# Kernel tuning notes

Hardware: AMD Instinct MI355X
Metric: run time of the kernel (lower is better)

## Reference

```python
import jax, jax.numpy as jnp
import numpy as np

N_NODES = 100000
N_EDGES = 1600000
D_IN = 128
D_OUT = 128
EPS = 1e-5


def setup_inputs() -> dict:
    key = jax.random.key(0)
    ks = jax.random.split(key, 5)
    x = jax.random.normal(ks[0], (N_NODES, D_IN), dtype=jnp.float32)
    edge_index = jax.random.randint(ks[1], (2, N_EDGES), 0, N_NODES, dtype=jnp.int64)
    scale = 1.0 / np.sqrt(D_IN)
    W_root = jax.random.normal(ks[2], (D_IN, D_OUT), dtype=jnp.float32) * scale
    W_rel = jax.random.normal(ks[3], (D_IN, D_OUT), dtype=jnp.float32) * scale
    b_rel = jax.random.normal(ks[4], (D_OUT,), dtype=jnp.float32) * 0.01
    gamma = jnp.ones((D_OUT,), dtype=jnp.float32)
    beta = jnp.zeros((D_OUT,), dtype=jnp.float32)
    return {"x": x, "edge_index": edge_index, "W_root": W_root, "W_rel": W_rel,
            "b_rel": b_rel, "gamma": gamma, "beta": beta}


def reference(x, edge_index, W_root, W_rel, b_rel, gamma, beta):
    # GraphConv: out = aggr(x_j) @ W_rel + b_rel + x @ W_root   (aggr = sum)
    src = edge_index[0]
    dst = edge_index[1]
    aggr = jax.ops.segment_sum(x[src], dst, num_segments=x.shape[0])  # [N, D_IN]
    h = aggr @ W_rel + b_rel + x @ W_root                              # [N, D_OUT]
    # NodeLevelBatchNorm (training mode: batch stats over node dim, biased var)
    mean = jnp.mean(h, axis=0)
    var = jnp.mean(jnp.square(h - mean), axis=0)
    h_norm = (h - mean) * jax.lax.rsqrt(var + EPS) * gamma + beta
    return jax.nn.relu(h_norm)
```

## Files before the change

### kernel.cpp

```cpp
#include <hip/hip_runtime.h>

#define N_NODES 100000
#define N_EDGES 1600000
#define D 128
#define NB 196
#define EPT 10
#define CHUNK 2560
#define BIN_BLOCKS 625
#define CVT_X_BLOCKS 6250
#define ZROW N_NODES

typedef __bf16 bf16x8 __attribute__((ext_vector_type(8)));
typedef float f32x4 __attribute__((ext_vector_type(4)));

__device__ __forceinline__ unsigned f2bf(float f) {
    unsigned u = __float_as_uint(f);
    return (u + 0x7fffu + ((u >> 16) & 1u)) >> 16;
}
__device__ __forceinline__ float bf_lo(unsigned u) { return __uint_as_float(u << 16); }
__device__ __forceinline__ float bf_hi(unsigned u) { return __uint_as_float(u & 0xffff0000u); }

__global__ __launch_bounds__(256) void prep_kernel(const float* __restrict__ x,
                                                   const float* __restrict__ Wrel,
                                                   const float* __restrict__ Wroot,
                                                   const int* __restrict__ ei,
                                                   unsigned short* __restrict__ x_bf,
                                                   unsigned short* __restrict__ Wt,
                                                   int* __restrict__ bcount) {
    __shared__ int h[256];
    int b = blockIdx.x;
    int t = threadIdx.x;
    if (b < CVT_X_BLOCKS) {
        size_t i = ((size_t)b * 256 + t) * 8;
        float4 v0 = *(const float4*)(x + i);
        float4 v1 = *(const float4*)(x + i + 4);
        uint4 p;
        p.x = f2bf(v0.x) | (f2bf(v0.y) << 16);
        p.y = f2bf(v0.z) | (f2bf(v0.w) << 16);
        p.z = f2bf(v1.x) | (f2bf(v1.y) << 16);
        p.w = f2bf(v1.z) | (f2bf(v1.w) << 16);
        *(uint4*)(x_bf + i) = p;
    } else if (b < CVT_X_BLOCKS + 128) {
        int c = b - CVT_X_BLOCKS;
        float v = (t < 128) ? Wrel[t * D + c] : Wroot[(t - 128) * D + c];
        Wt[c * 256 + t] = (unsigned short)f2bf(v);
    } else if (b == CVT_X_BLOCKS + 128) {
        if (t < 16) *(uint4*)(x_bf + (size_t)ZROW * D + t * 8) = make_uint4(0, 0, 0, 0);
    } else {
        int blk = b - (CVT_X_BLOCKS + 129);
        h[t] = 0;
        __syncthreads();
        int base = blk * CHUNK;
#pragma unroll
        for (int i = 0; i < EPT; ++i) {
            int dst = ei[N_EDGES + base + i * 256 + t];
            atomicAdd(&h[dst >> 9], 1);
        }
        __syncthreads();
        if (t < NB && h[t]) atomicAdd(&bcount[t], h[t]);
    }
}

__global__ __launch_bounds__(256) void bscan_kernel(const int* __restrict__ bcount,
                                                    int* __restrict__ bucket_base,
                                                    int* __restrict__ bcur) {
    __shared__ int s[256];
    int t = threadIdx.x;
    int v = (t < NB) ? bcount[t] : 0;
    s[t] = v;
    __syncthreads();
    for (int off = 1; off < 256; off <<= 1) {
        int a = (t >= off) ? s[t - off] : 0;
        __syncthreads();
        s[t] += a;
        __syncthreads();
    }
    int excl = s[t] - v;
    if (t < NB) {
        bucket_base[t] = excl;
        bcur[t] = excl;
    }
    if (t == NB) bucket_base[NB] = N_EDGES;
}

__global__ __launch_bounds__(256) void binify_kernel(const int* __restrict__ ei,
                                                     int* __restrict__ bcur,
                                                     unsigned* __restrict__ epk) {
    __shared__ int lhist[256];
    __shared__ int lstart[256];
    __shared__ int lfill[256];
    __shared__ int gbase[256];
    __shared__ uint2 stage[CHUNK];

    int t = threadIdx.x;
    int base = blockIdx.x * CHUNK;
    lhist[t] = 0;
    lfill[t] = 0;
    __syncthreads();

    int src[EPT], dst[EPT];
#pragma unroll
    for (int i = 0; i < EPT; ++i) {
        int e = base + i * 256 + t;
        src[i] = ei[e];
        dst[i] = ei[N_EDGES + e];
        atomicAdd(&lhist[dst[i] >> 9], 1);
    }
    __syncthreads();

    int v = lhist[t];
    lstart[t] = v;
    __syncthreads();
    for (int off = 1; off < 256; off <<= 1) {
        int a = (t >= off) ? lstart[t - off] : 0;
        __syncthreads();
        lstart[t] += a;
        __syncthreads();
    }
    int excl = lstart[t] - v;
    if (t < NB && v > 0) gbase[t] = atomicAdd(&bcur[t], v);
    __syncthreads();
    lstart[t] = excl;
    __syncthreads();

#pragma unroll
    for (int i = 0; i < EPT; ++i) {
        int b = dst[i] >> 9;
        int lp = atomicAdd(&lfill[b], 1);
        stage[lstart[b] + lp] = make_uint2((unsigned)src[i], (unsigned)dst[i]);
    }
    __syncthreads();

    for (int i = t; i < CHUNK; i += 256) {
        uint2 p = stage[i];
        int b = (int)(p.y >> 9);
        unsigned code = p.x | ((p.y & 511u) << 17);
        epk[gbase[b] + (i - lstart[b])] = code;
    }
}

__global__ __launch_bounds__(256) void place_kernel(const unsigned* __restrict__ epk,
                                                    const int* __restrict__ bucket_base,
                                                    int* __restrict__ rowstart,
                                                    int* __restrict__ srcs) {
    __shared__ int bufA[512];
    __shared__ int bufB[512];
    int b = blockIdx.x;
    int t = threadIdx.x;
    int pbeg = bucket_base[b];
    int pend = bucket_base[b + 1];

    bufA[t] = 0;
    bufA[t + 256] = 0;
    __syncthreads();
    for (int i = pbeg + t; i < pend; i += 256)
        atomicAdd(&bufA[epk[i] >> 17], 1);
    __syncthreads();

    for (int j = t; j < 512; j += 256) bufB[j] = j ? bufA[j - 1] : 0;
    __syncthreads();
    int* cur = bufB;
    int* nxt = bufA;
    for (int off = 1; off < 512; off <<= 1) {
        for (int j = t; j < 512; j += 256)
            nxt[j] = cur[j] + ((j >= off) ? cur[j - off] : 0);
        __syncthreads();
        int* tmp = cur; cur = nxt; nxt = tmp;
    }

    for (int j = t; j < 512; j += 256) {
        int gnode = (b << 9) + j;
        int val = pbeg + cur[j];
        if (gnode <= N_NODES) rowstart[gnode] = val;
        nxt[j] = val;
    }
    __syncthreads();

    for (int i = pbeg + t; i < pend; i += 256) {
        unsigned code = epk[i];
        int pos = atomicAdd(&nxt[code >> 17], 1);
        srcs[pos] = (int)(code & 0x1FFFFu);
    }
}

__global__ __launch_bounds__(256) void gather_kernel(const unsigned short* __restrict__ x_bf,
                                                     const int* __restrict__ rowstart,
                                                     const int* __restrict__ srcs,
                                                     unsigned short* __restrict__ aggr_bf) {
    int t = threadIdx.x;
    int node = blockIdx.x * 16 + (t >> 4);
    int l16 = t & 15;
    int begin = rowstart[node];
    int end = rowstart[node + 1];
    const unsigned short* xp = x_bf + l16 * 8;
    float a0 = 0.f, a1 = 0.f, a2 = 0.f, a3 = 0.f;
    float a4 = 0.f, a5 = 0.f, a6 = 0.f, a7 = 0.f;
    for (int e = begin; e < end; e += 8) {
        int idx[8];
#pragma unroll
        for (int i = 0; i < 8; ++i) {
            int ee = e + i;
            int ec = (ee < end) ? ee : (end - 1);
            int sv = srcs[ec];
            idx[i] = (ee < end) ? sv : ZROW;
        }
        uint4 u[8];
#pragma unroll
        for (int i = 0; i < 8; ++i) u[i] = *(const uint4*)(xp + (size_t)idx[i] * D);
#pragma unroll
        for (int i = 0; i < 8; ++i) {
            a0 += bf_lo(u[i].x);
            a1 += bf_hi(u[i].x);
            a2 += bf_lo(u[i].y);
            a3 += bf_hi(u[i].y);
            a4 += bf_lo(u[i].z);
            a5 += bf_hi(u[i].z);
            a6 += bf_lo(u[i].w);
            a7 += bf_hi(u[i].w);
        }
    }
    uint4 w;
    w.x = f2bf(a0) | (f2bf(a1) << 16);
    w.y = f2bf(a2) | (f2bf(a3) << 16);
    w.z = f2bf(a4) | (f2bf(a5) << 16);
    w.w = f2bf(a6) | (f2bf(a7) << 16);
    *(uint4*)(aggr_bf + (size_t)node * D + l16 * 8) = w;
}

__global__ __launch_bounds__(256) void gemm_mfma(const unsigned short* __restrict__ aggr_bf,
                                                 const unsigned short* __restrict__ x_bf,
                                                 const unsigned short* __restrict__ Wt,
                                                 const float* __restrict__ brel,
                                                 unsigned short* __restrict__ h_bf,
                                                 float* __restrict__ gsum,
                                                 float* __restrict__ gss) {
    __shared__ unsigned short Bf[2048 * 8];
    __shared__ float sbias[128];
    __shared__ float SredS[4][128];
    __shared__ float SredQ[4][128];

    const int t = threadIdx.x;
    const int wave = t >> 6;
    const int lane = t & 63;
    const int quad = lane >> 4;
    const int l16 = lane & 15;
    const int blockRow = blockIdx.x * 128;

    if (t < 128) sbias[t] = brel[t];

    f32x4 acc[2][8];
#pragma unroll
    for (int i = 0; i < 2; ++i)
#pragma unroll
        for (int j = 0; j < 8; ++j) acc[i][j] = (f32x4){0.f, 0.f, 0.f, 0.f};

    const int rowb = blockRow + wave * 32;

#pragma unroll
    for (int half = 0; half < 2; ++half) {
#pragma unroll
        for (int f = t; f < 2048; f += 256) {
            int kcl = f >> 9;
            int ct = (f >> 6) & 7;
            int ln = f & 63;
            int col = ct * 16 + (ln & 15);
            int kb = half * 128 + kcl * 32 + ((ln >> 4) << 3);
            *(uint4*)&Bf[f * 8] = *(const uint4*)(Wt + col * 256 + kb);
        }
        __syncthreads();

        const unsigned short* Asrc = half ? x_bf : aggr_bf;
#pragma unroll
        for (int kcl = 0; kcl < 4; ++kcl) {
            const int k0 = kcl * 32 + quad * 8;
            bf16x8 af0 = *(const bf16x8*)(Asrc + (size_t)(rowb + l16) * D + k0);
            bf16x8 af1 = *(const bf16x8*)(Asrc + (size_t)(rowb + 16 + l16) * D + k0);
#pragma unroll
            for (int ct = 0; ct < 8; ++ct) {
                bf16x8 bfrag = *(const bf16x8*)&Bf[((kcl * 8 + ct) * 64 + lane) * 8];
                acc[0][ct] = __builtin_amdgcn_mfma_f32_16x16x32_bf16(af0, bfrag, acc[0][ct], 0, 0, 0);
                acc[1][ct] = __builtin_amdgcn_mfma_f32_16x16x32_bf16(af1, bfrag, acc[1][ct], 0, 0, 0);
            }
        }
        if (half == 0) __syncthreads();
    }

    float csum[8], css[8];
#pragma unroll
    for (int ct = 0; ct < 8; ++ct) { csum[ct] = 0.f; css[ct] = 0.f; }

#pragma unroll
    for (int rt = 0; rt < 2; ++rt) {
#pragma unroll
        for (int ct = 0; ct < 8; ++ct) {
            int col = ct * 16 + l16;
            float bv = sbias[col];
#pragma unroll
            for (int reg = 0; reg < 4; ++reg) {
                int row = blockRow + wave * 32 + rt * 16 + quad * 4 + reg;
                if (row < N_NODES) {
                    float v = acc[rt][ct][reg] + bv;
                    h_bf[(size_t)row * D + col] = (unsigned short)f2bf(v);
                    csum[ct] += v;
                    css[ct] += v * v;
                }
            }
        }
    }
#pragma unroll
    for (int ct = 0; ct < 8; ++ct) {
        float s = csum[ct], q = css[ct];
        s += __shfl_xor(s, 16);
        s += __shfl_xor(s, 32);
        q += __shfl_xor(q, 16);
        q += __shfl_xor(q, 32);
        if (quad == 0) {
            SredS[wave][ct * 16 + l16] = s;
            SredQ[wave][ct * 16 + l16] = q;
        }
    }
    __syncthreads();
    if (t < 128) {
        float s = SredS[0][t] + SredS[1][t] + SredS[2][t] + SredS[3][t];
        float q = SredQ[0][t] + SredQ[1][t] + SredQ[2][t] + SredQ[3][t];
        unsafeAtomicAdd(&gsum[t], s);
        unsafeAtomicAdd(&gss[t], q);
    }
}

__global__ __launch_bounds__(256) void norm_kernel(const unsigned short* __restrict__ h_bf,
                                                   float* __restrict__ out,
                                                   const float* __restrict__ gsum,
                                                   const float* __restrict__ gss,
                                                   const float* __restrict__ gamma,
                                                   const float* __restrict__ beta) {
    __shared__ float sscale[128];
    __shared__ float sshift[128];
    int t = threadIdx.x;
    if (t < 128) {
        const float inv_n = 1.0f / (float)N_NODES;
        float mean = gsum[t] * inv_n;
        float var = gss[t] * inv_n - mean * mean;
        float rs = rsqrtf(var + 1e-5f);
        float sc = gamma[t] * rs;
        sscale[t] = sc;
        sshift[t] = beta[t] - mean * sc;
    }
    __syncthreads();
    size_t e = ((size_t)blockIdx.x * 256 + t) * 4;
    if (e >= (size_t)N_NODES * D) return;
    int c = (int)(e & 127);
    uint2 u = *(const uint2*)(h_bf + e);
    float4 v;
    v.x = fmaxf(bf_lo(u.x) * sscale[c + 0] + sshift[c + 0], 0.f);
    v.y = fmaxf(bf_hi(u.x) * sscale[c + 1] + sshift[c + 1], 0.f);
    v.z = fmaxf(bf_lo(u.y) * sscale[c + 2] + sshift[c + 2], 0.f);
    v.w = fmaxf(bf_hi(u.y) * sscale[c + 3] + sshift[c + 3], 0.f);
    *(float4*)(out + e) = v;
}

extern "C" void kernel_launch(void* const* d_in, const int* in_sizes, int n_in,
                              void* d_out, int out_size, void* d_ws, size_t ws_size,
                              hipStream_t stream) {
    const float* x     = (const float*)d_in[0];
    const int*   ei    = (const int*)d_in[1];
    const float* Wroot = (const float*)d_in[2];
    const float* Wrel  = (const float*)d_in[3];
    const float* brel  = (const float*)d_in[4];
    const float* gamma = (const float*)d_in[5];
    const float* beta  = (const float*)d_in[6];
    float* out = (float*)d_out;

    unsigned short* aggr_bf = (unsigned short*)d_ws;
    unsigned short* x_bf    = aggr_bf + (size_t)N_NODES * D;
    unsigned short* Wt      = x_bf + (size_t)(N_NODES + 1) * D;
    float* gsum  = (float*)(Wt + 128 * 256);
    float* gss   = gsum + 128;
    int* bcount  = (int*)(gss + 128);
    int* bucket_base = bcount + 256;
    int* bcur    = bucket_base + 256;
    int* rowstart = bcur + 256;
    unsigned* epk = (unsigned*)(rowstart + 100352);
    int* srcs    = (int*)(epk + N_EDGES);
    unsigned short* h_bf = (unsigned short*)epk;

    hipMemsetAsync(gsum, 0, 512 * sizeof(int), stream);

    prep_kernel<<<CVT_X_BLOCKS + 129 + BIN_BLOCKS, 256, 0, stream>>>(
        x, Wrel, Wroot, ei, x_bf, Wt, bcount);
    bscan_kernel<<<1, 256, 0, stream>>>(bcount, bucket_base, bcur);
    binify_kernel<<<BIN_BLOCKS, 256, 0, stream>>>(ei, bcur, epk);
    place_kernel<<<NB, 256, 0, stream>>>(epk, bucket_base, rowstart, srcs);
    gather_kernel<<<N_NODES / 16, 256, 0, stream>>>(x_bf, rowstart, srcs, aggr_bf);
    gemm_mfma<<<(N_NODES + 127) / 128, 256, 0, stream>>>(aggr_bf, x_bf, Wt, brel, h_bf, gsum, gss);
    norm_kernel<<<12500, 256, 0, stream>>>(h_bf, out, gsum, gss, gamma, beta);
}
```

Before: 282.9 us.

## Pad per-node edge lists to multiples of eight for vectorized gather

```diff
diff --git a/kernel.cpp b/kernel.cpp
--- a/kernel.cpp
+++ b/kernel.cpp
@@ -9,6 +9,7 @@
 #define BIN_BLOCKS 625
 #define CVT_X_BLOCKS 6250
 #define ZROW N_NODES
+#define PBK 13312
 
 typedef __bf16 bf16x8 __attribute__((ext_vector_type(8)));
 typedef float f32x4 __attribute__((ext_vector_type(4)));
@@ -141,72 +142,118 @@
 
 __global__ __launch_bounds__(256) void place_kernel(const unsigned* __restrict__ epk,
                                                     const int* __restrict__ bucket_base,
-                                                    int* __restrict__ rowstart,
+                                                    int* __restrict__ rbeg,
+                                                    int* __restrict__ rend,
                                                     int* __restrict__ srcs) {
-    __shared__ int bufA[512];
-    __shared__ int bufB[512];
+    __shared__ int cnt[512];
+    __shared__ int sA[512];
+    __shared__ int sB[512];
+    __shared__ int cursor[512];
     int b = blockIdx.x;
     int t = threadIdx.x;
     int pbeg = bucket_base[b];
     int pend = bucket_base[b + 1];
-
-    bufA[t] = 0;
-    bufA[t + 256] = 0;
+    int R = b * PBK;
+
+    cnt[t] = 0;
+    cnt[t + 256] = 0;
     __syncthreads();
     for (int i = pbeg + t; i < pend; i += 256)
-        atomicAdd(&bufA[epk[i] >> 17], 1);
-    __syncthreads();
-
-    for (int j = t; j < 512; j += 256) bufB[j] = j ? bufA[j - 1] : 0;
-    __syncthreads();
-    int* cur = bufB;
-    int* nxt = bufA;
+        atomicAdd(&cnt[epk[i] >> 17], 1);
+    __syncthreads();
+
+    for (int j = t; j < 512; j += 256) sA[j] = j ? ((cnt[j - 1] + 7) & ~7) : 0;
+    __syncthreads();
+    int* cur = sA;
+    int* nxt = sB;
     for (int off = 1; off < 512; off <<= 1) {
         for (int j = t; j < 512; j += 256)
             nxt[j] = cur[j] + ((j >= off) ? cur[j - off] : 0);
         __syncthreads();
-        int* tmp = cur; cur = nxt; nxt = tmp;
+        int* tm = cur; cur = nxt; nxt = tm;
     }
 
     for (int j = t; j < 512; j += 256) {
-        int gnode = (b << 9) + j;
-        int val = pbeg + cur[j];
-        if (gnode <= N_NODES) rowstart[gnode] = val;
-        nxt[j] = val;
+        int pj = (cnt[j] + 7) & ~7;
+        int s = R + cur[j];
+        int g = (b << 9) + j;
+        if (g < 100352) { rbeg[g] = s; rend[g] = s + pj; }
+        cursor[j] = s;
     }
     __syncthreads();
 
     for (int i = pbeg + t; i < pend; i += 256) {
         unsigned code = epk[i];
-        int pos = atomicAdd(&nxt[code >> 17], 1);
+        int pos = atomicAdd(&cursor[code >> 17], 1);
         srcs[pos] = (int)(code & 0x1FFFFu);
     }
+    __syncthreads();
+
+    for (int j = t; j < 512; j += 256) {
+        int endp = R + cur[j] + ((cnt[j] + 7) & ~7);
+        for (int p = cursor[j]; p < endp; ++p) srcs[p] = ZROW;
+    }
 }
 
 __global__ __launch_bounds__(256) void gather_kernel(const unsigned short* __restrict__ x_bf,
-                                                     const int* __restrict__ rowstart,
+                                                     const int* __restrict__ rbeg,
+                                                     const int* __restrict__ rend,
                                                      const int* __restrict__ srcs,
                                                      unsigned short* __restrict__ aggr_bf) {
     int t = threadIdx.x;
     int node = blockIdx.x * 16 + (t >> 4);
     int l16 = t & 15;
-    int begin = rowstart[node];
-    int end = rowstart[node + 1];
+    int e = rbeg[node];
+    int end = rend[node];
     const unsigned short* xp = x_bf + l16 * 8;
     float a0 = 0.f, a1 = 0.f, a2 = 0.f, a3 = 0.f;
     float a4 = 0.f, a5 = 0.f, a6 = 0.f, a7 = 0.f;
-    for (int e = begin; e < end; e += 8) {
-        int idx[8];
-#pragma unroll
-        for (int i = 0; i < 8; ++i) {
-            int ee = e + i;
-            int ec = (ee < end) ? ee : (end - 1);
-            int sv = srcs[ec];
-            idx[i] = (ee < end) ? sv : ZROW;
-        }
+    for (; e + 15 < end; e += 16) {
+        int4 s0 = *(const int4*)(srcs + e);
+        int4 s1 = *(const int4*)(srcs + e + 4);
+        int4 s2 = *(const int4*)(srcs + e + 8);
+        int4 s3 = *(const int4*)(srcs + e + 12);
+        uint4 u[16];
+        u[0]  = *(const uint4*)(xp + (size_t)s0.x * D);
+        u[1]  = *(const uint4*)(xp + (size_t)s0.y * D);
+        u[2]  = *(const uint4*)(xp + (size_t)s0.z * D);
+        u[3]  = *(const uint4*)(xp + (size_t)s0.w * D);
+        u[4]  = *(const uint4*)(xp + (size_t)s1.x * D);
+        u[5]  = *(const uint4*)(xp + (size_t)s1.y * D);
+        u[6]  = *(const uint4*)(xp + (size_t)s1.z * D);
+        u[7]  = *(const uint4*)(xp + (size_t)s1.w * D);
+        u[8]  = *(const uint4*)(xp + (size_t)s2.x * D);
+        u[9]  = *(const uint4*)(xp + (size_t)s2.y * D);
+        u[10] = *(const uint4*)(xp + (size_t)s2.z * D);
+        u[11] = *(const uint4*)(xp + (size_t)s2.w * D);
+        u[12] = *(const uint4*)(xp + (size_t)s3.x * D);
+        u[13] = *(const uint4*)(xp + (size_t)s3.y * D);
+        u[14] = *(const uint4*)(xp + (size_t)s3.z * D);
+        u[15] = *(const uint4*)(xp + (size_t)s3.w * D);
+#pragma unroll
+        for (int i = 0; i < 16; ++i) {
+            a0 += bf_lo(u[i].x);
+            a1 += bf_hi(u[i].x);
+            a2 += bf_lo(u[i].y);
+            a3 += bf_hi(u[i].y);
+            a4 += bf_lo(u[i].z);
+            a5 += bf_hi(u[i].z);
+            a6 += bf_lo(u[i].w);
+            a7 += bf_hi(u[i].w);
+        }
+    }
+    if (e < end) {
+        int4 s0 = *(const int4*)(srcs + e);
+        int4 s1 = *(const int4*)(srcs + e + 4);
         uint4 u[8];
-#pragma unroll
-        for (int i = 0; i < 8; ++i) u[i] = *(const uint4*)(xp + (size_t)idx[i] * D);
+        u[0] = *(const uint4*)(xp + (size_t)s0.x * D);
+        u[1] = *(const uint4*)(xp + (size_t)s0.y * D);
+        u[2] = *(const uint4*)(xp + (size_t)s0.z * D);
+        u[3] = *(const uint4*)(xp + (size_t)s0.w * D);
+        u[4] = *(const uint4*)(xp + (size_t)s1.x * D);
+        u[5] = *(const uint4*)(xp + (size_t)s1.y * D);
+        u[6] = *(const uint4*)(xp + (size_t)s1.z * D);
+        u[7] = *(const uint4*)(xp + (size_t)s1.w * D);
 #pragma unroll
         for (int i = 0; i < 8; ++i) {
             a0 += bf_lo(u[i].x);
@@ -379,8 +426,9 @@
     int* bcount  = (int*)(gss + 128);
     int* bucket_base = bcount + 256;
     int* bcur    = bucket_base + 256;
-    int* rowstart = bcur + 256;
-    unsigned* epk = (unsigned*)(rowstart + 100352);
+    int* rbeg    = bcur + 256;
+    int* rend    = rbeg + 100352;
+    unsigned* epk = (unsigned*)(rend + 100352);
     int* srcs    = (int*)(epk + N_EDGES);
     unsigned short* h_bf = (unsigned short*)epk;
 
@@ -390,8 +438,8 @@
         x, Wrel, Wroot, ei, x_bf, Wt, bcount);
     bscan_kernel<<<1, 256, 0, stream>>>(bcount, bucket_base, bcur);
     binify_kernel<<<BIN_BLOCKS, 256, 0, stream>>>(ei, bcur, epk);
-    place_kernel<<<NB, 256, 0, stream>>>(epk, bucket_base, rowstart, srcs);
-    gather_kernel<<<N_NODES / 16, 256, 0, stream>>>(x_bf, rowstart, srcs, aggr_bf);
+    place_kernel<<<NB, 256, 0, stream>>>(epk, bucket_base, rbeg, rend, srcs);
+    gather_kernel<<<N_NODES / 16, 256, 0, stream>>>(x_bf, rbeg, rend, srcs, aggr_bf);
     gemm_mfma<<<(N_NODES + 127) / 128, 256, 0, stream>>>(aggr_bf, x_bf, Wt, brel, h_bf, gsum, gss);
     norm_kernel<<<12500, 256, 0, stream>>>(h_bf, out, gsum, gss, gamma, beta);
 }
```

Result: no change. 287.7 us (+1.7%).
